# Optimization experiments

Measured on AMD Instinct MI355X. Metric: run time of the kernel, lower is better.

Reference implementation:

```python
import jax, jax.numpy as jnp
import numpy as np

N = 50000
IN_DIM, HID_DIM, OUT_DIM = 16, 64, 32


def setup_inputs() -> dict:
    key = jax.random.key(0)
    k1, k2, k3, k4, k5 = jax.random.split(key, 5)
    x = jax.random.normal(k1, (N, IN_DIM), dtype=jnp.float32)
    edge_index = jax.random.randint(k2, (2, 800000), 0, N, dtype=jnp.int64)
    # GCNConv weights (glorot-ish scale) and biases
    W1 = jax.random.normal(k3, (IN_DIM, HID_DIM), dtype=jnp.float32) / np.sqrt(IN_DIM)
    b1 = jnp.zeros((HID_DIM,), dtype=jnp.float32)
    W2 = jax.random.normal(k4, (HID_DIM, OUT_DIM), dtype=jnp.float32) / np.sqrt(HID_DIM)
    b2 = jnpplus = jnp.zeros((OUT_DIM,), dtype=jnp.float32)
    return {"x": x, "edge_index": edge_index, "W1": W1, "b1": b1, "W2": W2, "b2": b2}


def _gcn_conv(x, src, dst, norm, W, b, num_nodes):
    # PyG GCNConv: h = X W; out[d] = sum_e norm_e * h[src_e]; out += b
    h = x @ W                                   # [N, D_out] small GEMM
    msgs = h[src] * norm[:, None]               # [E+N, D_out] gather (memory-bound)
    out = jax.ops.segment_sum(msgs, dst, num_segments=num_nodes)  # scatter-add
    return out + b


def reference(x, edge_index, W1, b1, W2, b2):
    num_nodes = x.shape[0]
    # add self-loops (PyG GCNConv default add_self_loops=True)
    loops = jnp.arange(num_nodes, dtype=edge_index.dtype)
    src = jnp.concatenate([edge_index[0], loops])
    dst = jnp.concatenate([edge_index[1], loops])
    # symmetric normalization D^{-1/2} (A+I) D^{-1/2}, degree over dst
    deg = jax.ops.segment_sum(jnp.ones_like(src, dtype=x.dtype), dst, num_segments=num_nodes)
    dinv = jnp.where(deg > 0, jax.lax.rsqrt(deg), 0.0)
    norm = dinv[src] * dinv[dst]                # [E+N]

    h = _gcn_conv(x, src, dst, norm, W1, b1, num_nodes)
    h = jax.nn.relu(h)
    out = _gcn_conv(h, src, dst, norm, W2, b2, num_nodes)
    return out
```

## Files before the change

### kernel.cpp

```cpp
#include <hip/hip_runtime.h>
#include <hip/hip_fp16.h>

#define IN_DIM  16
#define HID_DIM 64
#define OUT_DIM 32

#define CAP 8192
#define EPB 3328

__device__ __forceinline__ int detect_is64(const void* edges) {
    const int* w = (const int*)edges;
    int is64 = 1;
    #pragma unroll
    for (int i = 0; i < 16; ++i) is64 &= (w[2 * i + 1] == 0);
    return is64;
}

__device__ __forceinline__ long long edge_at(const void* edges, int is64, long long i) {
    if (is64) return ((const long long*)edges)[i];
    return (long long)((const int*)edges)[i];
}

__global__ __launch_bounds__(256) void k_partA(const void* edges, int* gcur,
                                               unsigned int* gpart, int nbuk, long long E) {
    __shared__ unsigned int staged[EPB];
    __shared__ int hcnt[256], hoff[256], hcur[256];
    __shared__ int s64s;
    int t = threadIdx.x;
    if (t == 0) s64s = detect_is64(edges);
    hcnt[t] = 0;
    __syncthreads();
    int is64 = s64s;

    long long e0 = (long long)blockIdx.x * EPB;
    unsigned int rs[13], rd[13];
    int nval = 0;
    #pragma unroll
    for (int k = 0; k < 13; ++k) {
        long long e = e0 + t + k * 256;
        if (e < E) {
            rs[k] = (unsigned int)edge_at(edges, is64, e);
            rd[k] = (unsigned int)edge_at(edges, is64, E + e);
            atomicAdd(&hcnt[rd[k] >> 8], 1);
            nval = k + 1;
        }
    }
    __syncthreads();

    int v = hcnt[t];
    hoff[t] = v;
    __syncthreads();
    for (int d = 1; d < 256; d <<= 1) {
        int u = (t >= d) ? hoff[t - d] : 0;
        __syncthreads();
        hoff[t] += u;
        __syncthreads();
    }
    int excl = hoff[t] - v;
    hoff[t] = excl;
    hcur[t] = excl;
    __syncthreads();

    #pragma unroll
    for (int k = 0; k < 13; ++k) {
        if (k < nval) {
            int p = atomicAdd(&hcur[rd[k] >> 8], 1);
            staged[p] = rs[k] | ((rd[k] & 255u) << 16);
        }
    }
    __syncthreads();

    if (t < nbuk) {
        int c = hcnt[t];
        if (c > 0) {
            int base = atomicAdd(&gcur[t], c);
            int o = hoff[t];
            for (int k = 0; k < c; ++k) {
                int idx = base + k;
                if (idx < CAP) gpart[(size_t)t * CAP + idx] = staged[o + k];
            }
        }
    }
}

__global__ __launch_bounds__(256) void k_partB(const int* __restrict__ gcur,
                                               const unsigned int* __restrict__ gpart,
                                               unsigned int* __restrict__ csr,
                                               int* __restrict__ offs,
                                               int* __restrict__ degN,
                                               float* __restrict__ dinv,
                                               int nbuk, int N) {
    __shared__ unsigned int ebuf[CAP];
    __shared__ int bscan[256];
    __shared__ int hcnt[256], hoff[256], hcur[256];
    int t = threadIdx.x;
    int b = blockIdx.x;

    int bc = (t < nbuk) ? min(gcur[t], CAP) : 0;
    bscan[t] = bc;
    hcnt[t] = 0;
    __syncthreads();
    for (int d = 1; d < 256; d <<= 1) {
        int u = (t >= d) ? bscan[t - d] : 0;
        __syncthreads();
        bscan[t] += u;
        __syncthreads();
    }
    int base = (b == 0) ? 0 : bscan[b - 1];
    int cnt  = bscan[b] - base;

    for (int i = t; i < cnt; i += 256) ebuf[i] = gpart[(size_t)b * CAP + i];
    __syncthreads();
    for (int i = t; i < cnt; i += 256) atomicAdd(&hcnt[(ebuf[i] >> 16) & 255u], 1);
    __syncthreads();

    int v = hcnt[t];
    hoff[t] = v;
    __syncthreads();
    for (int d = 1; d < 256; d <<= 1) {
        int u = (t >= d) ? hoff[t - d] : 0;
        __syncthreads();
        hoff[t] += u;
        __syncthreads();
    }
    int excl = hoff[t] - v;
    hcur[t] = excl;
    __syncthreads();

    int node = b * 256 + t;
    if (node < N) {
        offs[node] = base + excl;
        degN[node] = v;
        dinv[node] = rsqrtf((float)v + 1.0f);
    }
    if (b == nbuk - 1 && t == 0) offs[N] = bscan[nbuk - 1];

    for (int i = t; i < cnt; i += 256) {
        unsigned int e = ebuf[i];
        int dl = (e >> 16) & 255;
        int p = atomicAdd(&hcur[dl], 1);
        csr[base + p] = e & 0xffffu;
    }
}

__global__ void k_finalize(unsigned int* csr, const int* __restrict__ degN, long long E) {
    long long j = blockIdx.x * 256LL + threadIdx.x;
    if (j >= E) return;
    unsigned int s = csr[j];
    csr[j] = s | ((unsigned int)min(degN[s], 65535) << 16);
}

__global__ __launch_bounds__(256) void k_agg1(
    const float* __restrict__ x, const float* __restrict__ dinv,
    const int* __restrict__ offs, const unsigned int* __restrict__ csr,
    float* __restrict__ aggX, int N)
{
    int node = (blockIdx.x * 256 + threadIdx.x) >> 6;
    if (node >= N) return;
    int lane = threadIdx.x & 63;
    int comp = lane & 3;
    int g    = lane >> 2;
    const float4* x4 = (const float4*)x;
    float di = dinv[node];
    int start = offs[node], end = offs[node + 1];
    float4 acc = make_float4(0.f, 0.f, 0.f, 0.f);
    if (g == 0) {
        float4 xs = x4[(size_t)node * 4 + comp];
        acc = make_float4(di * xs.x, di * xs.y, di * xs.z, di * xs.w);
    }
    for (int j = start + g; j < end; j += 16) {
        unsigned int p = csr[j];
        float w = rsqrtf((float)(p >> 16) + 1.0f);
        float4 xv = x4[(size_t)(p & 0xffffu) * 4 + comp];
        acc.x += w * xv.x; acc.y += w * xv.y;
        acc.z += w * xv.z; acc.w += w * xv.w;
    }
    #pragma unroll
    for (int m = 4; m < 64; m <<= 1) {
        acc.x += __shfl_xor(acc.x, m, 64);
        acc.y += __shfl_xor(acc.y, m, 64);
        acc.z += __shfl_xor(acc.z, m, 64);
        acc.w += __shfl_xor(acc.w, m, 64);
    }
    if (g == 0)
        ((float4*)aggX)[(size_t)node * 4 + comp] =
            make_float4(di * acc.x, di * acc.y, di * acc.z, di * acc.w);
}

#define AGG_P 20
#define H1_P  68
__global__ __launch_bounds__(256) void k_gemm12(
    const float* __restrict__ aggX,
    const float* __restrict__ W1, const float* __restrict__ b1,
    const float* __restrict__ W2, __half* __restrict__ h2, int N)
{
    __shared__ float W1s[IN_DIM * HID_DIM];
    __shared__ float W2s[HID_DIM * OUT_DIM];
    __shared__ float b1s[HID_DIM];
    __shared__ float aggs[64 * AGG_P];
    __shared__ float h1s[64 * H1_P];

    int tid = threadIdx.x;
    int base = blockIdx.x * 64;
    for (int i = tid; i < IN_DIM * HID_DIM; i += 256) W1s[i] = W1[i];
    for (int i = tid; i < HID_DIM * OUT_DIM; i += 256) W2s[i] = W2[i];
    if (tid < HID_DIM) b1s[tid] = b1[tid];

    {
        int node = tid >> 2, comp = tid & 3;
        float4 v = (base + node < N) ? ((const float4*)aggX)[(size_t)(base + node) * 4 + comp]
                                     : make_float4(0.f, 0.f, 0.f, 0.f);
        *(float4*)&aggs[node * AGG_P + comp * 4] = v;
    }
    __syncthreads();

    int node = tid >> 2, q = tid & 3;

    {
        float acc[16];
        #pragma unroll
        for (int c = 0; c < 16; ++c) acc[c] = b1s[q * 16 + c];
        #pragma unroll
        for (int k = 0; k < IN_DIM; ++k) {
            float a = aggs[node * AGG_P + k];
            const float4* wr = (const float4*)&W1s[k * HID_DIM + q * 16];
            #pragma unroll
            for (int c4 = 0; c4 < 4; ++c4) {
                float4 w = wr[c4];
                acc[c4 * 4 + 0] += a * w.x; acc[c4 * 4 + 1] += a * w.y;
                acc[c4 * 4 + 2] += a * w.z; acc[c4 * 4 + 3] += a * w.w;
            }
        }
        float4* h1row = (float4*)&h1s[node * H1_P + q * 16];
        #pragma unroll
        for (int c4 = 0; c4 < 4; ++c4)
            h1row[c4] = make_float4(fmaxf(acc[c4 * 4 + 0], 0.f), fmaxf(acc[c4 * 4 + 1], 0.f),
                                    fmaxf(acc[c4 * 4 + 2], 0.f), fmaxf(acc[c4 * 4 + 3], 0.f));
    }
    __syncthreads();

    {
        float acc2[8];
        #pragma unroll
        for (int c = 0; c < 8; ++c) acc2[c] = 0.f;
        const float4* h1row = (const float4*)&h1s[node * H1_P];
        #pragma unroll
        for (int k4 = 0; k4 < 16; ++k4) {
            float4 hv = h1row[k4];
            float hvv[4] = {hv.x, hv.y, hv.z, hv.w};
            #pragma unroll
            for (int kk = 0; kk < 4; ++kk) {
                int k = k4 * 4 + kk;
                const float4* wr = (const float4*)&W2s[k * OUT_DIM + q * 8];
                float4 w0 = wr[0], w1 = wr[1];
                acc2[0] += hvv[kk] * w0.x; acc2[1] += hvv[kk] * w0.y;
                acc2[2] += hvv[kk] * w0.z; acc2[3] += hvv[kk] * w0.w;
                acc2[4] += hvv[kk] * w1.x; acc2[5] += hvv[kk] * w1.y;
                acc2[6] += hvv[kk] * w1.z; acc2[7] += hvv[kk] * w1.w;
            }
        }
        if (base + node < N) {
            __half2 p[4];
            #pragma unroll
            for (int c = 0; c < 4; ++c)
                p[c] = __floats2half2_rn(acc2[c * 2], acc2[c * 2 + 1]);
            ((uint4*)h2)[(size_t)(base + node) * 4 + q] = *(uint4*)p;
        }
    }
}

__global__ __launch_bounds__(256) void k_agg2(
    const __half* __restrict__ h2, const float* __restrict__ dinv,
    const int* __restrict__ offs, const unsigned int* __restrict__ csr,
    const float* __restrict__ b2, float* __restrict__ out, int N)
{
    int node = (blockIdx.x * 256 + threadIdx.x) >> 6;
    if (node >= N) return;
    int lane = threadIdx.x & 63;
    int comp = lane & 3;
    int way  = lane >> 2;
    const uint4* h24 = (const uint4*)h2;
    float di = dinv[node];
    int start = offs[node], end = offs[node + 1];
    float acc[8] = {0.f, 0.f, 0.f, 0.f, 0.f, 0.f, 0.f, 0.f};
    if (way == 0) {
        uint4 r = h24[(size_t)node * 4 + comp];
        const __half2* hp = (const __half2*)&r;
        #pragma unroll
        for (int c = 0; c < 4; ++c) {
            float2 f = __half22float2(hp[c]);
            acc[c * 2]     = di * f.x;
            acc[c * 2 + 1] = di * f.y;
        }
    }
    for (int j = start + way; j < end; j += 16) {
        unsigned int p = csr[j];
        float w = rsqrtf((float)(p >> 16) + 1.0f);
        uint4 r = h24[(size_t)(p & 0xffffu) * 4 + comp];
        const __half2* hp = (const __half2*)&r;
        #pragma unroll
        for (int c = 0; c < 4; ++c) {
            float2 f = __half22float2(hp[c]);
            acc[c * 2]     += w * f.x;
            acc[c * 2 + 1] += w * f.y;
        }
    }
    #pragma unroll
    for (int m = 4; m < 64; m <<= 1) {
        #pragma unroll
        for (int c = 0; c < 8; ++c) acc[c] += __shfl_xor(acc[c], m, 64);
    }
    if (way == 0) {
        const float4* b24 = (const float4*)b2;
        float4 bb0 = b24[comp * 2], bb1 = b24[comp * 2 + 1];
        float4* out4 = (float4*)out;
        out4[(size_t)node * 8 + comp * 2 + 0] =
            make_float4(di * acc[0] + bb0.x, di * acc[1] + bb0.y,
                        di * acc[2] + bb0.z, di * acc[3] + bb0.w);
        out4[(size_t)node * 8 + comp * 2 + 1] =
            make_float4(di * acc[4] + bb1.x, di * acc[5] + bb1.y,
                        di * acc[6] + bb1.z, di * acc[7] + bb1.w);
    }
}

extern "C" void kernel_launch(void* const* d_in, const int* in_sizes, int n_in,
                              void* d_out, int out_size, void* d_ws, size_t ws_size,
                              hipStream_t stream) {
    const float* x     = (const float*)d_in[0];
    const void*  edges = d_in[1];
    const float* W1    = (const float*)d_in[2];
    const float* b1    = (const float*)d_in[3];
    const float* W2    = (const float*)d_in[4];
    const float* b2    = (const float*)d_in[5];
    float* out = (float*)d_out;

    const int       N = in_sizes[0] / IN_DIM;
    const long long E = in_sizes[1] / 2;
    const int    NBUK = (N + 255) >> 8;

    unsigned int* csr   = (unsigned int*)d_ws;
    unsigned int* gpart = csr + ((E + 3) & ~3LL);
    float*  aggX     = (float*)(gpart + (size_t)NBUK * CAP);
    __half* h2       = (__half*)(aggX + (size_t)IN_DIM * N);
    float*  dinv     = (float*)(h2 + (size_t)OUT_DIM * N);
    int*    offs     = (int*)(dinv + N);
    int*    degN     = offs + N + 1;
    int*    gcur     = degN + N;

    const int B = 256;
    hipMemsetAsync(gcur, 0, (size_t)NBUK * sizeof(int), stream);
    k_partA<<<(int)((E + EPB - 1) / EPB), B, 0, stream>>>(edges, gcur, gpart, NBUK, E);
    k_partB<<<NBUK, B, 0, stream>>>(gcur, gpart, csr, offs, degN, dinv, NBUK, N);
    k_finalize<<<(int)((E + B - 1) / B), B, 0, stream>>>(csr, degN, E);

    k_agg1<<<(N + 3) / 4, B, 0, stream>>>(x, dinv, offs, csr, aggX, N);
    k_gemm12<<<(N + 63) / 64, B, 0, stream>>>(aggX, W1, b1, W2, h2, N);
    k_agg2<<<(N + 3) / 4, B, 0, stream>>>(h2, dinv, offs, csr, b2, out, N);
}
```

Baseline: 154.6 us.

## Drop finalize pass; store 16-bit CSR sources and gather dinv directly

Removes the k_finalize kernel that packed each source's degree into the upper 16 bits of the CSR entries, along with the degN array. The CSR now holds only 16-bit source indices, which halves index traffic in both aggregation kernels. The per-edge weight is read from the dinv array (an extra random 4-byte gather) instead of being computed from the packed degree. The trade is one fewer launch and full pass over the edges against an extra gather per edge; dinv is 200KB and should be cache-resident. Source indices are still truncated to 16 bits, as before, even though N is 50000.

Result: faster. 148.6 us (-3.9%).

```diff
diff --git a/kernel.cpp b/kernel.cpp
--- a/kernel.cpp
+++ b/kernel.cpp
@@ -85,9 +85,8 @@
 
 __global__ __launch_bounds__(256) void k_partB(const int* __restrict__ gcur,
                                                const unsigned int* __restrict__ gpart,
-                                               unsigned int* __restrict__ csr,
+                                               unsigned short* __restrict__ csr,
                                                int* __restrict__ offs,
-                                               int* __restrict__ degN,
                                                float* __restrict__ dinv,
                                                int nbuk, int N) {
     __shared__ unsigned int ebuf[CAP];
@@ -130,7 +129,6 @@
     int node = b * 256 + t;
     if (node < N) {
         offs[node] = base + excl;
-        degN[node] = v;
         dinv[node] = rsqrtf((float)v + 1.0f);
     }
     if (b == nbuk - 1 && t == 0) offs[N] = bscan[nbuk - 1];
@@ -139,20 +137,13 @@
         unsigned int e = ebuf[i];
         int dl = (e >> 16) & 255;
         int p = atomicAdd(&hcur[dl], 1);
-        csr[base + p] = e & 0xffffu;
-    }
-}
-
-__global__ void k_finalize(unsigned int* csr, const int* __restrict__ degN, long long E) {
-    long long j = blockIdx.x * 256LL + threadIdx.x;
-    if (j >= E) return;
-    unsigned int s = csr[j];
-    csr[j] = s | ((unsigned int)min(degN[s], 65535) << 16);
+        csr[base + p] = (unsigned short)(e & 0xffffu);
+    }
 }
 
 __global__ __launch_bounds__(256) void k_agg1(
     const float* __restrict__ x, const float* __restrict__ dinv,
-    const int* __restrict__ offs, const unsigned int* __restrict__ csr,
+    const int* __restrict__ offs, const unsigned short* __restrict__ csr,
     float* __restrict__ aggX, int N)
 {
     int node = (blockIdx.x * 256 + threadIdx.x) >> 6;
@@ -169,9 +160,9 @@
         acc = make_float4(di * xs.x, di * xs.y, di * xs.z, di * xs.w);
     }
     for (int j = start + g; j < end; j += 16) {
-        unsigned int p = csr[j];
-        float w = rsqrtf((float)(p >> 16) + 1.0f);
-        float4 xv = x4[(size_t)(p & 0xffffu) * 4 + comp];
+        int s = csr[j];
+        float w = dinv[s];
+        float4 xv = x4[(size_t)s * 4 + comp];
         acc.x += w * xv.x; acc.y += w * xv.y;
         acc.z += w * xv.z; acc.w += w * xv.w;
     }
@@ -271,7 +262,7 @@
 
 __global__ __launch_bounds__(256) void k_agg2(
     const __half* __restrict__ h2, const float* __restrict__ dinv,
-    const int* __restrict__ offs, const unsigned int* __restrict__ csr,
+    const int* __restrict__ offs, const unsigned short* __restrict__ csr,
     const float* __restrict__ b2, float* __restrict__ out, int N)
 {
     int node = (blockIdx.x * 256 + threadIdx.x) >> 6;
@@ -294,9 +285,9 @@
         }
     }
     for (int j = start + way; j < end; j += 16) {
-        unsigned int p = csr[j];
-        float w = rsqrtf((float)(p >> 16) + 1.0f);
-        uint4 r = h24[(size_t)(p & 0xffffu) * 4 + comp];
+        int s = csr[j];
+        float w = dinv[s];
+        uint4 r = h24[(size_t)s * 4 + comp];
         const __half2* hp = (const __half2*)&r;
         #pragma unroll
         for (int c = 0; c < 4; ++c) {
@@ -338,20 +329,18 @@
     const long long E = in_sizes[1] / 2;
     const int    NBUK = (N + 255) >> 8;
 
-    unsigned int* csr   = (unsigned int*)d_ws;
-    unsigned int* gpart = csr + ((E + 3) & ~3LL);
+    unsigned short* csr   = (unsigned short*)d_ws;
+    unsigned int*   gpart = (unsigned int*)(csr + ((E + 7) & ~7LL));
     float*  aggX     = (float*)(gpart + (size_t)NBUK * CAP);
     __half* h2       = (__half*)(aggX + (size_t)IN_DIM * N);
     float*  dinv     = (float*)(h2 + (size_t)OUT_DIM * N);
     int*    offs     = (int*)(dinv + N);
-    int*    degN     = offs + N + 1;
-    int*    gcur     = degN + N;
+    int*    gcur     = offs + N + 1;
 
     const int B = 256;
     hipMemsetAsync(gcur, 0, (size_t)NBUK * sizeof(int), stream);
     k_partA<<<(int)((E + EPB - 1) / EPB), B, 0, stream>>>(edges, gcur, gpart, NBUK, E);
-    k_partB<<<NBUK, B, 0, stream>>>(gcur, gpart, csr, offs, degN, dinv, NBUK, N);
-    k_finalize<<<(int)((E + B - 1) / B), B, 0, stream>>>(csr, degN, E);
+    k_partB<<<NBUK, B, 0, stream>>>(gcur, gpart, csr, offs, dinv, NBUK, N);
 
     k_agg1<<<(N + 3) / 4, B, 0, stream>>>(x, dinv, offs, csr, aggX, N);
     k_gemm12<<<(N + 63) / 64, B, 0, stream>>>(aggX, W1, b1, W2, h2, N);
```
